# Kernel tuning notes

Measured on AMD Instinct MI355X. Metric: run time of the kernel, lower is better.

## Reference

```python
import jax, jax.numpy as jnp
import numpy as np

DIM = 256
NUM_HEADS = 4
HEAD_DIM = DIM // NUM_HEADS
LN_EPS = 1e-5


def setup_inputs() -> dict:
    key = jax.random.key(0)
    ks = jax.random.split(key, 5)
    B, C, H, W = 4, DIM, 64, 64
    x = jax.random.normal(ks[0], (B, C, H, W), dtype=jnp.float32)
    ln_g = jnp.ones((DIM,), dtype=jnp.float32)
    ln_b = jnp.zeros((DIM,), dtype=jnp.float32)
    # torch Linear init scale ~ 1/sqrt(fan_in)
    w_qkv = jax.random.normal(ks[1], (DIM, 3 * DIM), dtype=jnp.float32) / np.sqrt(DIM)
    w_proj = jax.random.normal(ks[2], (DIM, DIM), dtype=jnp.float32) / np.sqrt(DIM)
    b_proj = jax.random.normal(ks[3], (DIM,), dtype=jnp.float32) * 0.01
    return {"x": x, "ln_g": ln_g, "ln_b": ln_b, "w_qkv": w_qkv,
            "w_proj": w_proj, "b_proj": b_proj}


def _attention_block(x, ln_g, ln_b, w_qkv, w_proj, b_proj):
    B, C, H, W = x.shape
    N = H * W
    h, d = NUM_HEADS, HEAD_DIM
    # b c h w -> b n c
    t = x.reshape(B, C, N).transpose(0, 2, 1)
    # LayerNorm over channel dim
    mu = jnp.mean(t, axis=-1, keepdims=True)
    var = jnp.mean(jnp.square(t - mu), axis=-1, keepdims=True)
    t = (t - mu) * jax.lax.rsqrt(var + LN_EPS) * ln_g + ln_b
    # qkv projection (no bias); layout of last dim is (three, heads, d)
    qkv = t @ w_qkv  # [B, N, 3*C]
    qkv = qkv.reshape(B, N, 3, h, d)
    q = qkv[:, :, 0].transpose(0, 2, 1, 3)  # [B, h, N, d]
    k = qkv[:, :, 1].transpose(0, 2, 1, 3)
    v = qkv[:, :, 2].transpose(0, 2, 1, 3)
    # scaled dot-product attention (original chunks over queries; same math)
    scale = 1.0 / jnp.sqrt(jnp.asarray(d, dtype=q.dtype))
    dots = jnp.einsum('bhnd,bhmd->bhnm', q, k) * scale
    attn = jax.nn.softmax(dots, axis=-1)
    o = jnp.einsum('bhnm,bhmd->bhnd', attn, v)  # [B, h, N, d]
    # b h n d -> b n (h d)
    o = o.transpose(0, 2, 1, 3).reshape(B, N, C)
    o = o @ w_proj.T + b_proj  # torch Linear convention not needed; keep explicit
    # b n c -> b c h w
    return o.transpose(0, 2, 1).reshape(B, C, H, W)


def reference(x, ln_g, ln_b, w_qkv, w_proj, b_proj):
    return _attention_block(x, ln_g, ln_b, w_qkv, w_proj, b_proj)
```

## Files before the change

### kernel.cpp

```cpp
#include <hip/hip_runtime.h>
#include <math.h>

#define NB 4
#define NC 256
#define NHEADS 4
#define DH 64
#define NT 4096
#define QSCALE (0.125f * 1.44269504088896f)

typedef __bf16  bf16x8 __attribute__((ext_vector_type(8)));
typedef __bf16  bf16x4 __attribute__((ext_vector_type(4)));
typedef float   f32x4  __attribute__((ext_vector_type(4)));
typedef float   f32x16 __attribute__((ext_vector_type(16)));
typedef short   s16x8  __attribute__((ext_vector_type(8)));
typedef unsigned int u32x4 __attribute__((ext_vector_type(4)));

static __device__ __forceinline__ unsigned short f2bf(float f) {
    unsigned u = __float_as_uint(f);
    u = (u + 0x7fffu + ((u >> 16) & 1u)) >> 16;
    return (unsigned short)u;
}

static __device__ __forceinline__ float fast_exp2(float x) {
    return __builtin_amdgcn_exp2f(x);
}

static __device__ __forceinline__ unsigned cvtpk(float lo, float hi) {
    unsigned r;
    asm("v_cvt_pk_bf16_f32 %0, %1, %2" : "=v"(r) : "v"(lo), "v"(hi));
    return r;
}

static __device__ __forceinline__ void plswap(unsigned &a, unsigned &b) {
    asm("v_permlane32_swap_b32 %0, %1" : "+v"(a), "+v"(b));
}

static __device__ __forceinline__ bf16x8 as_bf16x8(u32x4 v) {
    return __builtin_bit_cast(bf16x8, v);
}

static __device__ __forceinline__ void gload16(const unsigned short* g, unsigned short* l) {
    __builtin_amdgcn_global_load_lds((const __attribute__((address_space(1))) void*)g,
                                     (__attribute__((address_space(3))) void*)l, 16, 0, 0);
}

static __device__ __forceinline__ void stage_64x256(
    unsigned short* __restrict__ lds, const unsigned short* __restrict__ g, int tid)
{
    #pragma unroll
    for (int chunk = 0; chunk < 8; ++chunk) {
        const int row = chunk * 8 + (tid >> 5);
        const int col = (tid & 31) * 8;
        *(s16x8*)&lds[row * 264 + col] = *(const s16x8*)&g[row * 256 + col];
    }
}

__global__ __launch_bounds__(256) void k_prep(
    const float* __restrict__ wqkv, const float* __restrict__ wproj,
    unsigned short* __restrict__ wqkv_t, unsigned short* __restrict__ wproj_bf)
{
    const int id = blockIdx.x;
    const int tid = threadIdx.x;
    if (id < 48) {
        __shared__ float T[64][65];
        const int jt = id % 12, ct = id / 12;
        #pragma unroll
        for (int p = 0; p < 16; ++p) {
            const int idx = tid + (p << 8);
            const int r = idx >> 6, cl = idx & 63;
            T[r][cl] = wqkv[(size_t)(ct * 64 + r) * 768 + jt * 64 + cl];
        }
        __syncthreads();
        #pragma unroll
        for (int p = 0; p < 16; ++p) {
            const int idx = tid + (p << 8);
            const int r = idx >> 6, cl = idx & 63;
            wqkv_t[(size_t)(jt * 64 + r) * 256 + ct * 64 + cl] = f2bf(T[cl][r]);
        }
    } else {
        const int base = (id - 48) * 2048 + tid * 8;
        s16x8 v;
        #pragma unroll
        for (int j = 0; j < 8; ++j) v[j] = (short)f2bf(wproj[base + j]);
        *(s16x8*)&wproj_bf[base] = v;
    }
}

__global__ __launch_bounds__(256) void k_ln_qkv(
    const float* __restrict__ x,
    const float* __restrict__ ln_g,
    const float* __restrict__ ln_b,
    const unsigned short* __restrict__ wqkv_t,
    unsigned short* __restrict__ q_bf,
    unsigned short* __restrict__ k_bf,
    unsigned short* __restrict__ v_bf)
{
    __shared__ unsigned short An[64 * 264];
    __shared__ unsigned short Wt[64 * 264];
    __shared__ float red1[4][64], red2[4][64];
    __shared__ float mu_s[64], rs_s[64];

    const int b     = blockIdx.x >> 6;
    const int n0    = (blockIdx.x & 63) << 6;
    const int three = blockIdx.y;
    const int tid   = threadIdx.x;
    const int li    = tid & 63;
    const int grp   = tid >> 6;
    const int w     = grp;
    const int lane  = li;
    const int q4    = lane >> 4;
    const int c     = lane & 15;

    const float* xb = x + ((size_t)b * NC) * NT + n0 + li;

    float xr[64];
    #pragma unroll
    for (int chunk = 0; chunk < 8; ++chunk)
        #pragma unroll
        for (int j = 0; j < 8; ++j)
            xr[chunk * 8 + j] = xb[(size_t)(chunk * 32 + grp * 8 + j) * NT];

    float s1 = 0.f, s2 = 0.f;
    #pragma unroll
    for (int i = 0; i < 64; ++i) { s1 += xr[i]; s2 += xr[i] * xr[i]; }
    red1[grp][li] = s1; red2[grp][li] = s2;
    __syncthreads();
    if (tid < 64) {
        const float t1 = red1[0][tid] + red1[1][tid] + red1[2][tid] + red1[3][tid];
        const float t2 = red2[0][tid] + red2[1][tid] + red2[2][tid] + red2[3][tid];
        const float mu  = t1 * (1.0f / NC);
        const float var = t2 * (1.0f / NC) - mu * mu;
        mu_s[tid] = mu;
        rs_s[tid] = rsqrtf(var + 1e-5f);
    }
    __syncthreads();
    const float mu = mu_s[li];
    const float rs = rs_s[li];

    #pragma unroll
    for (int chunk = 0; chunk < 8; ++chunk) {
        s16x8 pk;
        #pragma unroll
        for (int j = 0; j < 8; ++j) {
            const int ch = chunk * 32 + grp * 8 + j;
            const float vv = (xr[chunk * 8 + j] - mu) * rs * ln_g[ch] + ln_b[ch];
            pk[j] = (short)f2bf(vv);
        }
        *(s16x8*)&An[li * 264 + chunk * 32 + grp * 8] = pk;
    }
    __syncthreads();

    bf16x8 aT[8];
    if (three < 2) {
        #pragma unroll
        for (int kt = 0; kt < 8; ++kt)
            aT[kt] = *(const bf16x8*)&An[(16 * w + c) * 264 + kt * 32 + q4 * 8];
    }

    for (int jt = 0; jt < 4; ++jt) {
        __syncthreads();
        stage_64x256(Wt, wqkv_t + (size_t)(three * 256 + jt * 64) * 256, tid);
        __syncthreads();

        f32x4 acc[4];
        #pragma unroll
        for (int nt = 0; nt < 4; ++nt)
            #pragma unroll
            for (int r = 0; r < 4; ++r) acc[nt][r] = 0.f;

        const int bh = b * NHEADS + jt;
        if (three < 2) {
            #pragma unroll
            for (int nt = 0; nt < 4; ++nt)
                #pragma unroll
                for (int kt = 0; kt < 8; ++kt) {
                    const bf16x8 bb = *(const bf16x8*)&Wt[(16 * nt + c) * 264 + kt * 32 + q4 * 8];
                    acc[nt] = __builtin_amdgcn_mfma_f32_16x16x32_bf16(aT[kt], bb, acc[nt], 0, 0, 0);
                }
            unsigned short* dst = (three == 0 ? q_bf : k_bf) + ((size_t)bh * NT + n0) * DH;
            const float sc = (three == 0) ? QSCALE : 1.0f;
            #pragma unroll
            for (int nt = 0; nt < 4; ++nt)
                #pragma unroll
                for (int r = 0; r < 4; ++r)
                    dst[(size_t)(16 * w + 4 * q4 + r) * DH + 16 * nt + c] = f2bf(acc[nt][r] * sc);
        } else {
            bf16x8 aW[8];
            #pragma unroll
            for (int kt = 0; kt < 8; ++kt)
                aW[kt] = *(const bf16x8*)&Wt[(16 * w + c) * 264 + kt * 32 + q4 * 8];
            #pragma unroll
            for (int nt = 0; nt < 4; ++nt)
                #pragma unroll
                for (int kt = 0; kt < 8; ++kt) {
                    const bf16x8 bb = *(const bf16x8*)&An[(16 * nt + c) * 264 + kt * 32 + q4 * 8];
                    acc[nt] = __builtin_amdgcn_mfma_f32_16x16x32_bf16(aW[kt], bb, acc[nt], 0, 0, 0);
                }
            unsigned short* dst = v_bf + (size_t)bh * DH * NT;
            #pragma unroll
            for (int nt = 0; nt < 4; ++nt)
                #pragma unroll
                for (int r = 0; r < 4; ++r)
                    dst[(size_t)(16 * w + 4 * q4 + r) * NT + n0 + 16 * nt + c] = f2bf(acc[nt][r]);
        }
    }
}

__global__ __launch_bounds__(256, 4) void k_attn(
    const unsigned short* __restrict__ qg,
    const unsigned short* __restrict__ kg,
    const unsigned short* __restrict__ vg,
    float* __restrict__ o_part,
    float* __restrict__ l_part)
{
    __shared__ unsigned short Ks[2 * 4096];
    __shared__ unsigned short Vt[2 * 4096];

    const int bx   = ((blockIdx.x & 7) << 7) | (blockIdx.x >> 3);
    const int bh   = bx >> 6;
    const int qt   = (bx >> 1) & 31;
    const int kh   = bx & 1;
    const int n0   = qt << 7;
    const int tid  = threadIdx.x;
    const int w    = tid >> 6;
    const int lane = tid & 63;
    const int c5   = lane & 31;
    const int hi   = lane >> 5;
    const int qb   = n0 + (w << 5);

    const unsigned short* kb = kg + ((size_t)bh * NT + (kh << 11)) * DH;
    const unsigned short* vb = vg + (size_t)bh * DH * NT + (kh << 11);

    bf16x8 aq[4];
    {
        const unsigned short* qrow = qg + ((size_t)bh * NT + qb + c5) * DH + hi * 8;
        #pragma unroll
        for (int ks = 0; ks < 4; ++ks)
            aq[ks] = *(const bf16x8*)(qrow + ks * 16);
    }

    const int rr = lane >> 3;
    const int kc = (lane & 7) ^ rr;
    const int koffK = rr * DH + kc * 8;

    #define ISSUE_TILE(it_, bi_)                                               \
        {                                                                      \
            const unsigned short* ktp = kb + (size_t)(it_) * 64 * DH;          \
            const unsigned short* vtp = vb + (size_t)(it_) * 64;               \
            _Pragma("unroll")                                                  \
            for (int t = 0; t < 2; ++t) {                                      \
                const int grp_ = w * 2 + t;                                    \
                gload16(ktp + grp_ * 512 + koffK,                              \
                        &Ks[(bi_) * 4096 + grp_ * 512 + lane * 8]);            \
                gload16(vtp + (size_t)(grp_ * 8 + rr) * NT + kc * 8,           \
                        &Vt[(bi_) * 4096 + grp_ * 512 + lane * 8]);            \
            }                                                                  \
        }

    ISSUE_TILE(0, 0)

    f32x16 oac[2];
    #pragma unroll
    for (int dt = 0; dt < 2; ++dt)
        #pragma unroll
        for (int r = 0; r < 16; ++r) oac[dt][r] = 0.f;
    float lsum = 0.f;

    const int swz = (c5 & 7);

    for (int it = 0; it < 32; ++it) {
        const int cur = it & 1;
        asm volatile("s_waitcnt vmcnt(0)\n\ts_barrier" ::: "memory");
        if (it < 31) ISSUE_TILE(it + 1, cur ^ 1)

        const unsigned short* Kb = &Ks[cur * 4096];
        const unsigned short* Vb = &Vt[cur * 4096];

        #pragma unroll
        for (int sb = 0; sb < 2; ++sb) {
            f32x16 sacc;
            #pragma unroll
            for (int r = 0; r < 16; ++r) sacc[r] = 0.f;
            #pragma unroll
            for (int ks = 0; ks < 4; ++ks) {
                const bf16x8 kf = *(const bf16x8*)
                    &Kb[(sb * 32 + c5) * 64 + (((2 * ks + hi) ^ swz) << 3)];
                sacc = __builtin_amdgcn_mfma_f32_32x32x16_bf16(kf, aq[ks], sacc, 0, 0, 0);
            }

            #pragma unroll
            for (int r = 0; r < 16; ++r) {
                sacc[r] = fast_exp2(sacc[r]);
                lsum += sacc[r];
            }

            unsigned X0 = cvtpk(sacc[0],  sacc[1]);
            unsigned X1 = cvtpk(sacc[4],  sacc[5]);
            plswap(X0, X1);
            unsigned X2 = cvtpk(sacc[2],  sacc[3]);
            unsigned X3 = cvtpk(sacc[6],  sacc[7]);
            plswap(X2, X3);
            const u32x4 paA = (u32x4){X0, X2, X1, X3};

            unsigned Y0 = cvtpk(sacc[8],  sacc[9]);
            unsigned Y1 = cvtpk(sacc[12], sacc[13]);
            plswap(Y0, Y1);
            unsigned Y2 = cvtpk(sacc[10], sacc[11]);
            unsigned Y3 = cvtpk(sacc[14], sacc[15]);
            plswap(Y2, Y3);
            const u32x4 paB = (u32x4){Y0, Y2, Y1, Y3};

            #pragma unroll
            for (int dt = 0; dt < 2; ++dt) {
                const bf16x8 vA = *(const bf16x8*)
                    &Vb[(dt * 32 + c5) * 64 + (((4 * sb + hi) ^ swz) << 3)];
                oac[dt] = __builtin_amdgcn_mfma_f32_32x32x16_bf16(
                    as_bf16x8(paA), vA, oac[dt], 0, 0, 0);
                const bf16x8 vB = *(const bf16x8*)
                    &Vb[(dt * 32 + c5) * 64 + (((4 * sb + 2 + hi) ^ swz) << 3)];
                oac[dt] = __builtin_amdgcn_mfma_f32_32x32x16_bf16(
                    as_bf16x8(paB), vB, oac[dt], 0, 0, 0);
            }
        }
    }
    #undef ISSUE_TILE

    float* op = o_part + (((size_t)kh * 16 + bh) * NT + qb) * DH;
    #pragma unroll
    for (int dt = 0; dt < 2; ++dt)
        #pragma unroll
        for (int r = 0; r < 16; ++r) {
            const int qrow = (r & 3) + 8 * (r >> 2) + 4 * hi;
            op[(size_t)qrow * DH + 32 * dt + c5] = oac[dt][r];
        }

    float t = lsum + __shfl_xor(lsum, 32);
    if (lane < 32)
        l_part[((size_t)kh * 16 + bh) * NT + qb + c5] = t;
}

__global__ __launch_bounds__(256) void k_proj(
    const float* __restrict__ o_part,
    const float* __restrict__ l_part,
    const unsigned short* __restrict__ wproj_bf,
    const float* __restrict__ b_proj,
    float* __restrict__ out)
{
    __shared__ unsigned short Os[64 * 264];
    __shared__ unsigned short Ws[64 * 264];

    const int b   = blockIdx.x >> 6;
    const int n0  = (blockIdx.x & 63) << 6;
    const int yh  = blockIdx.y;
    const int tid = threadIdx.x;
    const int w   = tid >> 6;
    const int lane = tid & 63;
    const int q4  = lane >> 4;
    const int c   = lane & 15;

    const size_t OPS = (size_t)16 * NT * DH;
    const size_t LPS = (size_t)16 * NT;

    #pragma unroll
    for (int chunk = 0; chunk < 8; ++chunk) {
        const int row = chunk * 8 + (tid >> 5);
        const int col = (tid & 31) * 8;
        const int hd  = col >> 6;
        const int c64 = col & 63;
        const size_t tok = (size_t)(b * NHEADS + hd) * NT + n0 + row;
        const float rv = 1.0f / (l_part[tok] + l_part[LPS + tok]);
        const float* p0 = o_part + tok * DH + c64;
        const float* p1 = p0 + OPS;
        const f32x4 a0 = *(const f32x4*)p0;
        const f32x4 a1 = *(const f32x4*)(p0 + 4);
        const f32x4 b0 = *(const f32x4*)p1;
        const f32x4 b1 = *(const f32x4*)(p1 + 4);
        s16x8 pk;
        #pragma unroll
        for (int j = 0; j < 4; ++j) {
            pk[j]     = (short)f2bf((a0[j] + b0[j]) * rv);
            pk[4 + j] = (short)f2bf((a1[j] + b1[j]) * rv);
        }
        *(s16x8*)&Os[row * 264 + col] = pk;
    }

    for (int ct = 0; ct < 2; ++ct) {
        const int cg0 = (yh * 2 + ct) * 64;
        if (ct) __syncthreads();
        stage_64x256(Ws, wproj_bf + (size_t)cg0 * NC, tid);
        __syncthreads();

        bf16x8 a[8];
        #pragma unroll
        for (int kt = 0; kt < 8; ++kt)
            a[kt] = *(const bf16x8*)&Ws[(16 * w + c) * 264 + kt * 32 + q4 * 8];

        f32x4 acc[4];
        #pragma unroll
        for (int nt = 0; nt < 4; ++nt)
            #pragma unroll
            for (int r = 0; r < 4; ++r) acc[nt][r] = 0.f;

        #pragma unroll
        for (int nt = 0; nt < 4; ++nt)
            #pragma unroll
            for (int kt = 0; kt < 8; ++kt) {
                const bf16x8 bb = *(const bf16x8*)&Os[(16 * nt + c) * 264 + kt * 32 + q4 * 8];
                acc[nt] = __builtin_amdgcn_mfma_f32_16x16x32_bf16(a[kt], bb, acc[nt], 0, 0, 0);
            }

        #pragma unroll
        for (int nt = 0; nt < 4; ++nt)
            #pragma unroll
            for (int r = 0; r < 4; ++r) {
                const int cg = cg0 + 16 * w + 4 * q4 + r;
                out[((size_t)b * NC + cg) * NT + n0 + 16 * nt + c] = acc[nt][r] + b_proj[cg];
            }
    }
}

extern "C" void kernel_launch(void* const* d_in, const int* in_sizes, int n_in,
                              void* d_out, int out_size, void* d_ws, size_t ws_size,
                              hipStream_t stream)
{
    const float* x      = (const float*)d_in[0];
    const float* ln_g   = (const float*)d_in[1];
    const float* ln_b   = (const float*)d_in[2];
    const float* w_qkv  = (const float*)d_in[3];
    const float* w_proj = (const float*)d_in[4];
    const float* b_proj = (const float*)d_in[5];
    float* out = (float*)d_out;

    const size_t TEN = (size_t)NB * NHEADS * NT * DH;

    float* ws32 = (float*)d_ws;
    float* o_part = ws32;
    float* l_part = ws32 + 8388608;
    unsigned short* ws16 = (unsigned short*)(l_part + 131072);
    unsigned short* q_bf    = ws16;
    unsigned short* k_bf    = ws16 + TEN;
    unsigned short* v_bf    = ws16 + 2 * TEN;
    unsigned short* wqkv_t  = ws16 + 3 * TEN;
    unsigned short* wproj_b = wqkv_t + 768 * 256;

    k_prep<<<80, 256, 0, stream>>>(w_qkv, w_proj, wqkv_t, wproj_b);
    k_ln_qkv<<<dim3(NB * 64, 3), 256, 0, stream>>>(x, ln_g, ln_b, wqkv_t, q_bf, k_bf, v_bf);
    k_attn<<<16 * 64, 256, 0, stream>>>(q_bf, k_bf, v_bf, o_part, l_part);
    k_proj<<<dim3(NB * 64, 2), 256, 0, stream>>>(o_part, l_part, wproj_b, b_proj, out);
}
```

Baseline: 194.1 us.

## Drop split-KV in attention, normalize in-kernel and emit bf16 output

The attention kernel no longer splits the key range into two halves with fp32 partial outputs and partial row sums merged in the projection kernel. Each block now covers the full key range with 128-key tiles, finishes the softmax normalization itself, and writes a bf16 output that k_proj loads directly. This removes the fp32 partial-output traffic and the merge work. It also adds s_setprio around the MFMA groups and splits the row-sum accumulation into four independent chains. In exchange the grid is halved to 512 blocks, LDS per block doubles and the occupancy hint drops from 4 to 2, so there is less parallelism to hide latency.

```diff
diff --git a/kernel.cpp b/kernel.cpp
--- a/kernel.cpp
+++ b/kernel.cpp
@@ -9,7 +9,6 @@
 #define QSCALE (0.125f * 1.44269504088896f)
 
 typedef __bf16  bf16x8 __attribute__((ext_vector_type(8)));
-typedef __bf16  bf16x4 __attribute__((ext_vector_type(4)));
 typedef float   f32x4  __attribute__((ext_vector_type(4)));
 typedef float   f32x16 __attribute__((ext_vector_type(16)));
 typedef short   s16x8  __attribute__((ext_vector_type(8)));
@@ -206,20 +205,19 @@
     }
 }
 
-__global__ __launch_bounds__(256, 4) void k_attn(
+__global__ __launch_bounds__(256, 2) void k_attn(
     const unsigned short* __restrict__ qg,
     const unsigned short* __restrict__ kg,
     const unsigned short* __restrict__ vg,
-    float* __restrict__ o_part,
-    float* __restrict__ l_part)
-{
-    __shared__ unsigned short Ks[2 * 4096];
-    __shared__ unsigned short Vt[2 * 4096];
-
-    const int bx   = ((blockIdx.x & 7) << 7) | (blockIdx.x >> 3);
-    const int bh   = bx >> 6;
-    const int qt   = (bx >> 1) & 31;
-    const int kh   = bx & 1;
+    unsigned short* __restrict__ og)
+{
+    __shared__ unsigned short Ks[2 * 8192];
+    __shared__ unsigned short Vt[2 * 8192];
+    __shared__ float l_s[4][32];
+
+    const int bx   = ((blockIdx.x & 7) << 6) | (blockIdx.x >> 3);
+    const int bh   = bx >> 5;
+    const int qt   = bx & 31;
     const int n0   = qt << 7;
     const int tid  = threadIdx.x;
     const int w    = tid >> 6;
@@ -227,9 +225,10 @@
     const int c5   = lane & 31;
     const int hi   = lane >> 5;
     const int qb   = n0 + (w << 5);
-
-    const unsigned short* kb = kg + ((size_t)bh * NT + (kh << 11)) * DH;
-    const unsigned short* vb = vg + (size_t)bh * DH * NT + (kh << 11);
+    const int swz  = c5 & 7;
+
+    const unsigned short* kb = kg + (size_t)bh * NT * DH;
+    const unsigned short* vb = vg + (size_t)bh * DH * NT;
 
     bf16x8 aq[4];
     {
@@ -239,21 +238,23 @@
             aq[ks] = *(const bf16x8*)(qrow + ks * 16);
     }
 
-    const int rr = lane >> 3;
-    const int kc = (lane & 7) ^ rr;
-    const int koffK = rr * DH + kc * 8;
+    const int rr  = lane >> 3;
+    const int kcK = (lane & 7) ^ rr;
+    const int rd  = lane >> 4;
+    const int ckV = lane & 15;
 
     #define ISSUE_TILE(it_, bi_)                                               \
         {                                                                      \
-            const unsigned short* ktp = kb + (size_t)(it_) * 64 * DH;          \
-            const unsigned short* vtp = vb + (size_t)(it_) * 64;               \
+            const unsigned short* ktp = kb + (size_t)(it_) * 128 * DH;         \
+            const unsigned short* vtp = vb + (size_t)(it_) * 128;              \
             _Pragma("unroll")                                                  \
-            for (int t = 0; t < 2; ++t) {                                      \
-                const int grp_ = w * 2 + t;                                    \
-                gload16(ktp + grp_ * 512 + koffK,                              \
-                        &Ks[(bi_) * 4096 + grp_ * 512 + lane * 8]);            \
-                gload16(vtp + (size_t)(grp_ * 8 + rr) * NT + kc * 8,           \
-                        &Vt[(bi_) * 4096 + grp_ * 512 + lane * 8]);            \
+            for (int t = 0; t < 4; ++t) {                                      \
+                const int grp_ = w * 4 + t;                                    \
+                gload16(ktp + (size_t)(grp_ * 8 + rr) * DH + kcK * 8,          \
+                        &Ks[(bi_) * 8192 + grp_ * 512 + lane * 8]);            \
+                const int kcV_ = ckV ^ ((4 * grp_ + rd) & 7);                  \
+                gload16(vtp + (size_t)(4 * grp_ + rd) * NT + kcV_ * 8,         \
+                        &Vt[(bi_) * 8192 + grp_ * 512 + lane * 8]);            \
             }                                                                  \
         }
 
@@ -264,84 +265,113 @@
     for (int dt = 0; dt < 2; ++dt)
         #pragma unroll
         for (int r = 0; r < 16; ++r) oac[dt][r] = 0.f;
-    float lsum = 0.f;
-
-    const int swz = (c5 & 7);
+    float ls0 = 0.f, ls1 = 0.f, ls2 = 0.f, ls3 = 0.f;
 
     for (int it = 0; it < 32; ++it) {
         const int cur = it & 1;
         asm volatile("s_waitcnt vmcnt(0)\n\ts_barrier" ::: "memory");
         if (it < 31) ISSUE_TILE(it + 1, cur ^ 1)
 
-        const unsigned short* Kb = &Ks[cur * 4096];
-        const unsigned short* Vb = &Vt[cur * 4096];
-
-        #pragma unroll
-        for (int sb = 0; sb < 2; ++sb) {
-            f32x16 sacc;
-            #pragma unroll
-            for (int r = 0; r < 16; ++r) sacc[r] = 0.f;
+        const unsigned short* Kb = &Ks[cur * 8192];
+        const unsigned short* Vb = &Vt[cur * 8192];
+
+        #pragma unroll
+        for (int hf = 0; hf < 2; ++hf) {
+            const int sb0 = 2 * hf, sb1 = 2 * hf + 1;
+
+            f32x16 s0, s1;
+            #pragma unroll
+            for (int r = 0; r < 16; ++r) { s0[r] = 0.f; s1[r] = 0.f; }
+            __builtin_amdgcn_s_setprio(1);
             #pragma unroll
             for (int ks = 0; ks < 4; ++ks) {
-                const bf16x8 kf = *(const bf16x8*)
-                    &Kb[(sb * 32 + c5) * 64 + (((2 * ks + hi) ^ swz) << 3)];
-                sacc = __builtin_amdgcn_mfma_f32_32x32x16_bf16(kf, aq[ks], sacc, 0, 0, 0);
-            }
-
-            #pragma unroll
-            for (int r = 0; r < 16; ++r) {
-                sacc[r] = fast_exp2(sacc[r]);
-                lsum += sacc[r];
-            }
-
-            unsigned X0 = cvtpk(sacc[0],  sacc[1]);
-            unsigned X1 = cvtpk(sacc[4],  sacc[5]);
-            plswap(X0, X1);
-            unsigned X2 = cvtpk(sacc[2],  sacc[3]);
-            unsigned X3 = cvtpk(sacc[6],  sacc[7]);
-            plswap(X2, X3);
-            const u32x4 paA = (u32x4){X0, X2, X1, X3};
-
-            unsigned Y0 = cvtpk(sacc[8],  sacc[9]);
-            unsigned Y1 = cvtpk(sacc[12], sacc[13]);
-            plswap(Y0, Y1);
-            unsigned Y2 = cvtpk(sacc[10], sacc[11]);
-            unsigned Y3 = cvtpk(sacc[14], sacc[15]);
-            plswap(Y2, Y3);
-            const u32x4 paB = (u32x4){Y0, Y2, Y1, Y3};
-
+                const bf16x8 kf0 = *(const bf16x8*)
+                    &Kb[(sb0 * 32 + c5) * 64 + (((2 * ks + hi) ^ swz) << 3)];
+                s0 = __builtin_amdgcn_mfma_f32_32x32x16_bf16(kf0, aq[ks], s0, 0, 0, 0);
+            }
+            #pragma unroll
+            for (int ks = 0; ks < 4; ++ks) {
+                const bf16x8 kf1 = *(const bf16x8*)
+                    &Kb[(sb1 * 32 + c5) * 64 + (((2 * ks + hi) ^ swz) << 3)];
+                s1 = __builtin_amdgcn_mfma_f32_32x32x16_bf16(kf1, aq[ks], s1, 0, 0, 0);
+            }
+            __builtin_amdgcn_s_setprio(0);
+
+            #pragma unroll
+            for (int r = 0; r < 16; r += 4) {
+                s0[r]   = fast_exp2(s0[r]);   ls0 += s0[r];
+                s0[r+1] = fast_exp2(s0[r+1]); ls1 += s0[r+1];
+                s0[r+2] = fast_exp2(s0[r+2]); ls2 += s0[r+2];
+                s0[r+3] = fast_exp2(s0[r+3]); ls3 += s0[r+3];
+            }
+            #pragma unroll
+            for (int r = 0; r < 16; r += 4) {
+                s1[r]   = fast_exp2(s1[r]);   ls0 += s1[r];
+                s1[r+1] = fast_exp2(s1[r+1]); ls1 += s1[r+1];
+                s1[r+2] = fast_exp2(s1[r+2]); ls2 += s1[r+2];
+                s1[r+3] = fast_exp2(s1[r+3]); ls3 += s1[r+3];
+            }
+
+            unsigned A0 = cvtpk(s0[0],  s0[1]),  A1 = cvtpk(s0[4],  s0[5]);
+            plswap(A0, A1);
+            unsigned A2 = cvtpk(s0[2],  s0[3]),  A3 = cvtpk(s0[6],  s0[7]);
+            plswap(A2, A3);
+            const u32x4 paA0 = (u32x4){A0, A2, A1, A3};
+            unsigned B0 = cvtpk(s0[8],  s0[9]),  B1 = cvtpk(s0[12], s0[13]);
+            plswap(B0, B1);
+            unsigned B2 = cvtpk(s0[10], s0[11]), B3 = cvtpk(s0[14], s0[15]);
+            plswap(B2, B3);
+            const u32x4 paB0 = (u32x4){B0, B2, B1, B3};
+            unsigned C0 = cvtpk(s1[0],  s1[1]),  C1 = cvtpk(s1[4],  s1[5]);
+            plswap(C0, C1);
+            unsigned C2 = cvtpk(s1[2],  s1[3]),  C3 = cvtpk(s1[6],  s1[7]);
+            plswap(C2, C3);
+            const u32x4 paA1 = (u32x4){C0, C2, C1, C3};
+            unsigned D0 = cvtpk(s1[8],  s1[9]),  D1 = cvtpk(s1[12], s1[13]);
+            plswap(D0, D1);
+            unsigned D2 = cvtpk(s1[10], s1[11]), D3 = cvtpk(s1[14], s1[15]);
+            plswap(D2, D3);
+            const u32x4 paB1 = (u32x4){D0, D2, D1, D3};
+
+            __builtin_amdgcn_s_setprio(1);
             #pragma unroll
             for (int dt = 0; dt < 2; ++dt) {
-                const bf16x8 vA = *(const bf16x8*)
-                    &Vb[(dt * 32 + c5) * 64 + (((4 * sb + hi) ^ swz) << 3)];
+                const int rv = (dt * 32 + c5) * 128;
+                const bf16x8 vA0 = *(const bf16x8*)&Vb[rv + (((4*sb0 + hi) ^ swz) << 3)];
                 oac[dt] = __builtin_amdgcn_mfma_f32_32x32x16_bf16(
-                    as_bf16x8(paA), vA, oac[dt], 0, 0, 0);
-                const bf16x8 vB = *(const bf16x8*)
-                    &Vb[(dt * 32 + c5) * 64 + (((4 * sb + 2 + hi) ^ swz) << 3)];
+                    as_bf16x8(paA0), vA0, oac[dt], 0, 0, 0);
+                const bf16x8 vB0 = *(const bf16x8*)&Vb[rv + (((4*sb0 + 2 + hi) ^ swz) << 3)];
                 oac[dt] = __builtin_amdgcn_mfma_f32_32x32x16_bf16(
-                    as_bf16x8(paB), vB, oac[dt], 0, 0, 0);
-            }
+                    as_bf16x8(paB0), vB0, oac[dt], 0, 0, 0);
+                const bf16x8 vA1 = *(const bf16x8*)&Vb[rv + (((4*sb1 + hi) ^ swz) << 3)];
+                oac[dt] = __builtin_amdgcn_mfma_f32_32x32x16_bf16(
+                    as_bf16x8(paA1), vA1, oac[dt], 0, 0, 0);
+                const bf16x8 vB1 = *(const bf16x8*)&Vb[rv + (((4*sb1 + 2 + hi) ^ swz) << 3)];
+                oac[dt] = __builtin_amdgcn_mfma_f32_32x32x16_bf16(
+                    as_bf16x8(paB1), vB1, oac[dt], 0, 0, 0);
+            }
+            __builtin_amdgcn_s_setprio(0);
         }
     }
     #undef ISSUE_TILE
 
-    float* op = o_part + (((size_t)kh * 16 + bh) * NT + qb) * DH;
-    #pragma unroll
-    for (int dt = 0; dt < 2; ++dt)
-        #pragma unroll
-        for (int r = 0; r < 16; ++r) {
-            const int qrow = (r & 3) + 8 * (r >> 2) + 4 * hi;
-            op[(size_t)qrow * DH + 32 * dt + c5] = oac[dt][r];
-        }
-
-    float t = lsum + __shfl_xor(lsum, 32);
-    if (lane < 32)
-        l_part[((size_t)kh * 16 + bh) * NT + qb + c5] = t;
+    const float lsum = (ls0 + ls1) + (ls2 + ls3);
+    const float t = lsum + __shfl_xor(lsum, 32);
+    if (lane < 32) l_s[w][c5] = t;
+    __syncthreads();
+
+    unsigned short* ob = og + ((size_t)bh * NT + qb) * DH;
+    #pragma unroll
+    for (int r = 0; r < 16; ++r) {
+        const int qrow = (r & 3) + 8 * (r >> 2) + 4 * hi;
+        const float rn = 1.0f / l_s[w][qrow];
+        ob[(size_t)qrow * DH + c5]      = f2bf(oac[0][r] * rn);
+        ob[(size_t)qrow * DH + 32 + c5] = f2bf(oac[1][r] * rn);
+    }
 }
 
 __global__ __launch_bounds__(256) void k_proj(
-    const float* __restrict__ o_part,
-    const float* __restrict__ l_part,
+    const unsigned short* __restrict__ o_bf,
     const unsigned short* __restrict__ wproj_bf,
     const float* __restrict__ b_proj,
     float* __restrict__ out)
@@ -358,30 +388,15 @@
     const int q4  = lane >> 4;
     const int c   = lane & 15;
 
-    const size_t OPS = (size_t)16 * NT * DH;
-    const size_t LPS = (size_t)16 * NT;
-
     #pragma unroll
     for (int chunk = 0; chunk < 8; ++chunk) {
         const int row = chunk * 8 + (tid >> 5);
         const int col = (tid & 31) * 8;
         const int hd  = col >> 6;
         const int c64 = col & 63;
-        const size_t tok = (size_t)(b * NHEADS + hd) * NT + n0 + row;
-        const float rv = 1.0f / (l_part[tok] + l_part[LPS + tok]);
-        const float* p0 = o_part + tok * DH + c64;
-        const float* p1 = p0 + OPS;
-        const f32x4 a0 = *(const f32x4*)p0;
-        const f32x4 a1 = *(const f32x4*)(p0 + 4);
-        const f32x4 b0 = *(const f32x4*)p1;
-        const f32x4 b1 = *(const f32x4*)(p1 + 4);
-        s16x8 pk;
-        #pragma unroll
-        for (int j = 0; j < 4; ++j) {
-            pk[j]     = (short)f2bf((a0[j] + b0[j]) * rv);
-            pk[4 + j] = (short)f2bf((a1[j] + b1[j]) * rv);
-        }
-        *(s16x8*)&Os[row * 264 + col] = pk;
+        const unsigned short* src =
+            &o_bf[((size_t)(b * NHEADS + hd) * NT + n0 + row) * DH + c64];
+        *(s16x8*)&Os[row * 264 + col] = *(const s16x8*)src;
     }
 
     for (int ct = 0; ct < 2; ++ct) {
@@ -433,18 +448,16 @@
 
     const size_t TEN = (size_t)NB * NHEADS * NT * DH;
 
-    float* ws32 = (float*)d_ws;
-    float* o_part = ws32;
-    float* l_part = ws32 + 8388608;
-    unsigned short* ws16 = (unsigned short*)(l_part + 131072);
+    unsigned short* ws16 = (unsigned short*)d_ws;
     unsigned short* q_bf    = ws16;
     unsigned short* k_bf    = ws16 + TEN;
     unsigned short* v_bf    = ws16 + 2 * TEN;
-    unsigned short* wqkv_t  = ws16 + 3 * TEN;
+    unsigned short* o_bf    = ws16 + 3 * TEN;
+    unsigned short* wqkv_t  = ws16 + 4 * TEN;
     unsigned short* wproj_b = wqkv_t + 768 * 256;
 
     k_prep<<<80, 256, 0, stream>>>(w_qkv, w_proj, wqkv_t, wproj_b);
     k_ln_qkv<<<dim3(NB * 64, 3), 256, 0, stream>>>(x, ln_g, ln_b, wqkv_t, q_bf, k_bf, v_bf);
-    k_attn<<<16 * 64, 256, 0, stream>>>(q_bf, k_bf, v_bf, o_part, l_part);
-    k_proj<<<dim3(NB * 64, 2), 256, 0, stream>>>(o_part, l_part, wproj_b, b_proj, out);
-}
+    k_attn<<<512, 256, 0, stream>>>(q_bf, k_bf, v_bf, o_bf);
+    k_proj<<<dim3(NB * 64, 2), 256, 0, stream>>>(o_bf, wproj_b, b_proj, out);
+}
```

Result: faster. 181.8 us (-6.4%).
